# Performance work log

Hardware: AMD Instinct MI355X
Metric: run time of the kernel (lower is better)

The kernel has to match this reference:

```python
import jax, jax.numpy as jnp
from jax import lax
import numpy as np

SLOPE = 0.1  # LeakyReLU negative slope used throughout DA_conv


def setup_inputs() -> dict:
    key = jax.random.key(0)
    ks = jax.random.split(key, 8)
    B, C, H, W = 16, 64, 160, 160
    Cout, red = 64, 8
    feat = jax.random.normal(ks[0], (B, C, H, W), dtype=jnp.float32)
    deg = jax.random.normal(ks[1], (B, C, 1, 1), dtype=jnp.float32)
    W1 = jax.random.normal(ks[2], (64, C), dtype=jnp.float32) * 0.05
    W2 = jax.random.normal(ks[3], (Cout * 9, 64), dtype=jnp.float32) * 0.05
    Wc = jax.random.normal(ks[4], (Cout, Cout), dtype=jnp.float32) * 0.05
    bc = jnp.zeros((Cout,), dtype=jnp.float32)
    Wd1 = jax.random.normal(ks[5], (red, C), dtype=jnp.float32) * 0.05
    Wd2 = jax.random.normal(ks[6], (Cout, red), dtype=jnp.float32) * 0.05
    return {"feat": feat, "deg": deg, "W1": W1, "W2": W2, "Wc": Wc,
            "bc": bc, "Wd1": Wd1, "Wd2": Wd2}


def reference(feat, deg, W1, W2, Wc, bc, Wd1, Wd2):
    B, C, H, W = feat.shape
    Cout = Wc.shape[0]
    KS = 3
    d = deg[:, :, 0, 0]  # [B, C]

    # --- dynamic per-sample, per-channel 3x3 kernel generation ---
    h = jax.nn.leaky_relu(d @ W1.T, SLOPE)            # [B, 64]
    k = (h @ W2.T).reshape(B * Cout, 1, KS, KS)        # [B*Cout, 1, 3, 3]

    # grouped depthwise conv: input [1, B*C, H, W], groups = B*C
    x = feat.reshape(1, B * C, H, W)
    out = lax.conv_general_dilated(
        x, k, window_strides=(1, 1), padding=[(1, 1), (1, 1)],
        dimension_numbers=("NCHW", "OIHW", "NCHW"),
        feature_group_count=B * C)
    out = jax.nn.leaky_relu(out, SLOPE).reshape(B, Cout, H, W)

    # 1x1 conv with bias (common.default_conv)
    out = jnp.einsum("oi,bihw->bohw", Wc, out) + bc[None, :, None, None]

    # --- channel attention branch (1x1 convs == matmuls on [B,C]) ---
    a = jax.nn.leaky_relu(jnp.einsum("ri,bi->br", Wd1, d), SLOPE)   # [B, red]
    att = jax.nn.sigmoid(jnp.einsum("or,br->bo", Wd2, a))           # [B, Cout]

    return out + feat * att[:, :, None, None]
```

## Files before the change

### kernel.cpp

```cpp
#include <hip/hip_runtime.h>
#include <hip/hip_bf16.h>
#include <math.h>

#define SLOPE 0.1f
#define B_ 16
#define C_ 64
#define H_ 160
#define W_ 160
#define HW_ (H_*W_)

typedef short bf16x8 __attribute__((ext_vector_type(8)));
typedef float f32x4  __attribute__((ext_vector_type(4)));
typedef unsigned int uint2v __attribute__((ext_vector_type(2)));

__device__ __forceinline__ float lrelu(float x) { return fmaxf(x, SLOPE * x); }
__device__ __forceinline__ unsigned f2bf(float x) {
  union { float f; unsigned u; } c; c.f = x;
  return (c.u + 0x7fffu + ((c.u >> 16) & 1u)) >> 16;
}
__device__ __forceinline__ float bf2f(unsigned short u) {
  union { unsigned u; float f; } c; c.u = ((unsigned)u) << 16; return c.f;
}

__device__ __forceinline__ void gl2lds16(const void* g, void* l) {
  __builtin_amdgcn_global_load_lds(
      (const __attribute__((address_space(1))) void*)g,
      (__attribute__((address_space(3))) void*)l, 16, 0, 0);
}

__global__ __launch_bounds__(64) void prep_kernel(
    const float* __restrict__ deg,
    const float* __restrict__ W1,
    const float* __restrict__ W2,
    const float* __restrict__ Wd1,
    const float* __restrict__ Wd2,
    float* __restrict__ ws) {
  const int b = blockIdx.x;
  const int j = threadIdx.x;
  __shared__ float sd[64], sh[64], sa[8];
  sd[j] = deg[b * 64 + j];
  __syncthreads();

  float acc = 0.f;
  for (int i = 0; i < 64; ++i) acc = fmaf(sd[i], W1[j * 64 + i], acc);
  sh[j] = lrelu(acc);

  if (j < 8) {
    float s = 0.f;
    for (int i = 0; i < 64; ++i) s = fmaf(sd[i], Wd1[j * 64 + i], s);
    sa[j] = lrelu(s);
  }
  __syncthreads();

  float kv[9];
#pragma unroll
  for (int t = 0; t < 9; ++t) kv[t] = 0.f;
  for (int l = 0; l < 64; ++l) {
    float hl = sh[l];
#pragma unroll
    for (int t = 0; t < 9; ++t) kv[t] = fmaf(hl, W2[(j * 9 + t) * 64 + l], kv[t]);
  }
  const int slot = ((j & 15) >> 2) * 16 + (j >> 4) * 4 + (j & 3);
  unsigned short* kw = (unsigned short*)((char*)ws + 4096) + (b * 64 + slot) * 12;
#pragma unroll
  for (int t = 0; t < 9; ++t) kw[t] = (unsigned short)f2bf(kv[t]);
  kw[9] = 0; kw[10] = 0; kw[11] = 0;

  float s2 = 0.f;
#pragma unroll
  for (int r = 0; r < 8; ++r) s2 = fmaf(Wd2[j * 8 + r], sa[r], s2);
  ws[b * 64 + j] = 1.f / (1.f + __expf(-s2));
}

__global__ __launch_bounds__(256, 4) void main_kernel(
    const float* __restrict__ feat,
    const float* __restrict__ Wc,
    const float* __restrict__ bc,
    const float* __restrict__ ws,
    float* __restrict__ out) {
  __shared__ __align__(16) float S[2][16][244];
  __shared__ __align__(16) unsigned short Tt[2048];
  __shared__ __align__(16) unsigned short Ff[2048];
  __shared__ __align__(16) unsigned short Kl[768];

  const int rb  = blockIdx.x;
  const int bid = (rb & 7) * 400 + (rb >> 3);
  const int b   = bid / 200;
  const int rem = bid - b * 200;
  const int ty  = rem / 10, tx = rem - ty * 10;
  const int x0 = tx * 16, y0 = ty * 8;
  const int tid = threadIdx.x;
  const int lane = tid & 63, wid = tid >> 6;

  const float* __restrict__ attp  = ws + b * 64;
  const char*  __restrict__ kb8   = (const char*)ws + 4096 + b * 1536;
  const float* __restrict__ plane = feat + (size_t)(b * 64) * HW_;

  const int ci = tid >> 4;
  const int q  = (tid >> 2) & 3;
  const int h  = tid & 3;
  const int nl = lane & 15, kg = lane >> 4;
  const int ochunk = wid * 16;

  const int srow = lane / 6;
  const int schk = lane - srow * 6;
  const int grow = min(max(y0 + srow - 1, 0), H_ - 1);
  const int gcol = min(max(x0 - 4 + schk * 4, 0), W_ - 4);
  const float* sp0 = plane + grow * W_ + gcol;

  union AF { bf16x8 v; unsigned short u[8]; };
  AF a[4];
  const unsigned short ab = (unsigned short)f2bf(attp[ochunk + nl]);
#pragma unroll
  for (int g = 0; g < 4; ++g) {
    const float4 w = *(const float4*)(Wc + (ochunk + nl) * 64 + g * 16 + 4 * kg);
    a[g].u[0] = (unsigned short)f2bf(w.x); a[g].u[1] = (unsigned short)f2bf(w.y);
    a[g].u[2] = (unsigned short)f2bf(w.z); a[g].u[3] = (unsigned short)f2bf(w.w);
#pragma unroll
    for (int j = 0; j < 4; ++j)
      a[g].u[4 + j] = (wid == g && nl == 4 * kg + j) ? ab : (unsigned short)0;
  }
  const float4 bcv = *(const float4*)(bc + ochunk + 4 * kg);

  asm volatile("s_waitcnt vmcnt(0)" ::: "memory");

  if (lane < 24) gl2lds16(kb8 + wid * 384 + lane * 16, &Kl[wid * 192]);
#define STAGE(g_, bf_) \
  if (lane < 60) { \
    const float* s_ = sp0 + (size_t)((g_) * 16 + wid * 4) * HW_; \
    gl2lds16(s_,            &S[bf_][wid * 4 + 0][0]); \
    gl2lds16(s_ + HW_,      &S[bf_][wid * 4 + 1][0]); \
    gl2lds16(s_ + 2 * HW_,  &S[bf_][wid * 4 + 2][0]); \
    gl2lds16(s_ + 3 * HW_,  &S[bf_][wid * 4 + 3][0]); \
  }
  STAGE(0, 0);
  STAGE(1, 1);

  f32x4 acc[8];
#pragma unroll
  for (int nt = 0; nt < 8; ++nt) acc[nt] = (f32x4){0.f, 0.f, 0.f, 0.f};

  const float mlz = (x0 == 0 && q == 0) ? 0.f : 1.f;
  const float mrz = (x0 == W_ - 16 && q == 3) ? 0.f : 1.f;

  const unsigned t_base = (unsigned)(uintptr_t)&Tt[0] + (unsigned)(lane * 8);
  const unsigned f_base = (unsigned)(uintptr_t)&Ff[0] + (unsigned)(lane * 8);
  union BU { bf16x8 v; uint2v qv[2]; };

#pragma unroll
  for (int g = 0; g < 4; ++g) {
    const int sb = g & 1;
    if (g < 3) {
      asm volatile("s_waitcnt vmcnt(4)" ::: "memory");
    } else {
      asm volatile("s_waitcnt vmcnt(0)" ::: "memory");
    }
    __builtin_amdgcn_sched_barrier(0);

    const unsigned short* kr = &Kl[(wid * 16 + g * 4 + (lane >> 4)) * 12];
    union KU { uint2v v; unsigned short u[4]; };
    KU kA, kB;
    kA.v = *(const uint2v*)(kr);
    kB.v = *(const uint2v*)(kr + 4);
    const unsigned short k8u = kr[8];
    float kk[9];
#pragma unroll
    for (int t = 0; t < 4; ++t) { kk[t] = bf2f(kA.u[t]); kk[4 + t] = bf2f(kB.u[t]); }
    kk[8] = bf2f(k8u);

    float rv[4][9];
#pragma unroll
    for (int rr = 0; rr < 4; ++rr) {
      const float* sp = &S[sb][ci][(2 * h + rr) * 24 + 4 * q];
      const f32x4 v0 = *(const f32x4*)sp;
      const f32x4 v1 = *(const f32x4*)(sp + 4);
      rv[rr][0] = v0[0]; rv[rr][1] = v0[1]; rv[rr][2] = v0[2];
      rv[rr][3] = v0[3] * mlz;
      rv[rr][4] = v1[0]; rv[rr][5] = v1[1]; rv[rr][6] = v1[2]; rv[rr][7] = v1[3];
      rv[rr][8] = sp[8] * mrz;
    }

#pragma unroll
    for (int rr = 0; rr < 2; ++rr) {
      const int srw = 2 * h + rr;
      const float mt = (srw == 0 && y0 == 0) ? 0.f : 1.f;
      const float mb = (srw == 7 && y0 == H_ - 8) ? 0.f : 1.f;
      float sv[4], fv[4];
#pragma unroll
      for (int j = 0; j < 4; ++j) {
        float ts = fmaf(rv[rr][j + 5], kk[2], fmaf(rv[rr][j + 4], kk[1], rv[rr][j + 3] * kk[0]));
        float cs = fmaf(rv[rr + 1][j + 5], kk[5], fmaf(rv[rr + 1][j + 4], kk[4], rv[rr + 1][j + 3] * kk[3]));
        float bs = fmaf(rv[rr + 2][j + 5], kk[8], fmaf(rv[rr + 2][j + 4], kk[7], rv[rr + 2][j + 3] * kk[6]));
        sv[j] = fmaf(mt, ts, fmaf(mb, bs, cs));
        fv[j] = rv[rr + 1][j + 4];
      }
      uint2v tq, fq;
      tq.x = f2bf(lrelu(sv[0])) | (f2bf(lrelu(sv[1])) << 16);
      tq.y = f2bf(lrelu(sv[2])) | (f2bf(lrelu(sv[3])) << 16);
      fq.x = f2bf(fv[0]) | (f2bf(fv[1]) << 16);
      fq.y = f2bf(fv[2]) | (f2bf(fv[3]) << 16);
      const int tidx = srw * 256 + ci * 16 + 4 * q;
      *(uint2v*)&Tt[tidx] = tq;
      *(uint2v*)&Ff[tidx] = fq;
    }

    if (g < 2) { STAGE(g + 2, sb); }

    asm volatile("s_waitcnt lgkmcnt(0)" ::: "memory");
    __builtin_amdgcn_sched_barrier(0);
    __builtin_amdgcn_s_barrier();
    __builtin_amdgcn_sched_barrier(0);

    if (wid == g) {
      uint2v t0, t1, t2, t3, t4, t5, t6, t7;
      uint2v f0, f1, f2, f3, f4, f5, f6, f7;
      asm volatile("ds_read_b64_tr_b16 %0, %1 offset:0"    : "=v"(t0) : "v"(t_base));
      asm volatile("ds_read_b64_tr_b16 %0, %1 offset:512"  : "=v"(t1) : "v"(t_base));
      asm volatile("ds_read_b64_tr_b16 %0, %1 offset:0"    : "=v"(f0) : "v"(f_base));
      asm volatile("ds_read_b64_tr_b16 %0, %1 offset:512"  : "=v"(f1) : "v"(f_base));
      asm volatile("ds_read_b64_tr_b16 %0, %1 offset:1024" : "=v"(t2) : "v"(t_base));
      asm volatile("ds_read_b64_tr_b16 %0, %1 offset:1536" : "=v"(t3) : "v"(t_base));
      asm volatile("ds_read_b64_tr_b16 %0, %1 offset:1024" : "=v"(f2) : "v"(f_base));
      asm volatile("ds_read_b64_tr_b16 %0, %1 offset:1536" : "=v"(f3) : "v"(f_base));
      asm volatile("s_waitcnt lgkmcnt(4)" ::: "memory");
      __builtin_amdgcn_sched_barrier(0);
      {
        BU u0, u1;
        u0.qv[0] = t0; u0.qv[1] = f0;
        u1.qv[0] = t1; u1.qv[1] = f1;
        acc[0] = __builtin_amdgcn_mfma_f32_16x16x32_bf16(a[g].v, u0.v, acc[0], 0, 0, 0);
        acc[1] = __builtin_amdgcn_mfma_f32_16x16x32_bf16(a[g].v, u1.v, acc[1], 0, 0, 0);
      }
      asm volatile("ds_read_b64_tr_b16 %0, %1 offset:2048" : "=v"(t4) : "v"(t_base));
      asm volatile("ds_read_b64_tr_b16 %0, %1 offset:2560" : "=v"(t5) : "v"(t_base));
      asm volatile("ds_read_b64_tr_b16 %0, %1 offset:2048" : "=v"(f4) : "v"(f_base));
      asm volatile("ds_read_b64_tr_b16 %0, %1 offset:2560" : "=v"(f5) : "v"(f_base));
      asm volatile("s_waitcnt lgkmcnt(4)" ::: "memory");
      __builtin_amdgcn_sched_barrier(0);
      {
        BU u2, u3;
        u2.qv[0] = t2; u2.qv[1] = f2;
        u3.qv[0] = t3; u3.qv[1] = f3;
        acc[2] = __builtin_amdgcn_mfma_f32_16x16x32_bf16(a[g].v, u2.v, acc[2], 0, 0, 0);
        acc[3] = __builtin_amdgcn_mfma_f32_16x16x32_bf16(a[g].v, u3.v, acc[3], 0, 0, 0);
      }
      asm volatile("ds_read_b64_tr_b16 %0, %1 offset:3072" : "=v"(t6) : "v"(t_base));
      asm volatile("ds_read_b64_tr_b16 %0, %1 offset:3584" : "=v"(t7) : "v"(t_base));
      asm volatile("ds_read_b64_tr_b16 %0, %1 offset:3072" : "=v"(f6) : "v"(f_base));
      asm volatile("ds_read_b64_tr_b16 %0, %1 offset:3584" : "=v"(f7) : "v"(f_base));
      asm volatile("s_waitcnt lgkmcnt(4)" ::: "memory");
      __builtin_amdgcn_sched_barrier(0);
      {
        BU u4, u5;
        u4.qv[0] = t4; u4.qv[1] = f4;
        u5.qv[0] = t5; u5.qv[1] = f5;
        acc[4] = __builtin_amdgcn_mfma_f32_16x16x32_bf16(a[g].v, u4.v, acc[4], 0, 0, 0);
        acc[5] = __builtin_amdgcn_mfma_f32_16x16x32_bf16(a[g].v, u5.v, acc[5], 0, 0, 0);
      }
      asm volatile("s_waitcnt lgkmcnt(0)" ::: "memory");
      __builtin_amdgcn_sched_barrier(0);
      {
        BU u6, u7;
        u6.qv[0] = t6; u6.qv[1] = f6;
        u7.qv[0] = t7; u7.qv[1] = f7;
        acc[6] = __builtin_amdgcn_mfma_f32_16x16x32_bf16(a[g].v, u6.v, acc[6], 0, 0, 0);
        acc[7] = __builtin_amdgcn_mfma_f32_16x16x32_bf16(a[g].v, u7.v, acc[7], 0, 0, 0);
      }
    } else {
      uint2v ta0, ta1, ta2, ta3, tb0, tb1, tb2, tb3;
      asm volatile("ds_read_b64_tr_b16 %0, %1 offset:0"    : "=v"(ta0) : "v"(t_base));
      asm volatile("ds_read_b64_tr_b16 %0, %1 offset:512"  : "=v"(ta1) : "v"(t_base));
      asm volatile("ds_read_b64_tr_b16 %0, %1 offset:1024" : "=v"(ta2) : "v"(t_base));
      asm volatile("ds_read_b64_tr_b16 %0, %1 offset:1536" : "=v"(ta3) : "v"(t_base));
      asm volatile("s_waitcnt lgkmcnt(0)" ::: "memory");
      __builtin_amdgcn_sched_barrier(0);
      asm volatile("ds_read_b64_tr_b16 %0, %1 offset:2048" : "=v"(tb0) : "v"(t_base));
      asm volatile("ds_read_b64_tr_b16 %0, %1 offset:2560" : "=v"(tb1) : "v"(t_base));
      asm volatile("ds_read_b64_tr_b16 %0, %1 offset:3072" : "=v"(tb2) : "v"(t_base));
      asm volatile("ds_read_b64_tr_b16 %0, %1 offset:3584" : "=v"(tb3) : "v"(t_base));
      {
        BU u0, u1, u2, u3;
        u0.qv[0] = ta0; u0.qv[1] = (uint2v){0u, 0u};
        u1.qv[0] = ta1; u1.qv[1] = (uint2v){0u, 0u};
        u2.qv[0] = ta2; u2.qv[1] = (uint2v){0u, 0u};
        u3.qv[0] = ta3; u3.qv[1] = (uint2v){0u, 0u};
        acc[0] = __builtin_amdgcn_mfma_f32_16x16x32_bf16(a[g].v, u0.v, acc[0], 0, 0, 0);
        acc[1] = __builtin_amdgcn_mfma_f32_16x16x32_bf16(a[g].v, u1.v, acc[1], 0, 0, 0);
        acc[2] = __builtin_amdgcn_mfma_f32_16x16x32_bf16(a[g].v, u2.v, acc[2], 0, 0, 0);
        acc[3] = __builtin_amdgcn_mfma_f32_16x16x32_bf16(a[g].v, u3.v, acc[3], 0, 0, 0);
      }
      asm volatile("s_waitcnt lgkmcnt(0)" ::: "memory");
      __builtin_amdgcn_sched_barrier(0);
      {
        BU u4, u5, u6, u7;
        u4.qv[0] = tb0; u4.qv[1] = (uint2v){0u, 0u};
        u5.qv[0] = tb1; u5.qv[1] = (uint2v){0u, 0u};
        u6.qv[0] = tb2; u6.qv[1] = (uint2v){0u, 0u};
        u7.qv[0] = tb3; u7.qv[1] = (uint2v){0u, 0u};
        acc[4] = __builtin_amdgcn_mfma_f32_16x16x32_bf16(a[g].v, u4.v, acc[4], 0, 0, 0);
        acc[5] = __builtin_amdgcn_mfma_f32_16x16x32_bf16(a[g].v, u5.v, acc[5], 0, 0, 0);
        acc[6] = __builtin_amdgcn_mfma_f32_16x16x32_bf16(a[g].v, u6.v, acc[6], 0, 0, 0);
        acc[7] = __builtin_amdgcn_mfma_f32_16x16x32_bf16(a[g].v, u7.v, acc[7], 0, 0, 0);
      }
    }
    __builtin_amdgcn_s_barrier();
    __builtin_amdgcn_sched_barrier(0);
  }
#undef STAGE

  const int ob = ochunk + 4 * kg;
  float* __restrict__ outb = out + (size_t)(b * 64) * HW_;
#pragma unroll
  for (int nt = 0; nt < 8; ++nt) {
    const int off = (y0 + nt) * W_ + x0 + nl;
    outb[(size_t)(ob + 0) * HW_ + off] = acc[nt][0] + bcv.x;
    outb[(size_t)(ob + 1) * HW_ + off] = acc[nt][1] + bcv.y;
    outb[(size_t)(ob + 2) * HW_ + off] = acc[nt][2] + bcv.z;
    outb[(size_t)(ob + 3) * HW_ + off] = acc[nt][3] + bcv.w;
  }
}

extern "C" void kernel_launch(void* const* d_in, const int* in_sizes, int n_in,
                              void* d_out, int out_size, void* d_ws, size_t ws_size,
                              hipStream_t stream) {
  const float* feat = (const float*)d_in[0];
  const float* deg  = (const float*)d_in[1];
  const float* W1   = (const float*)d_in[2];
  const float* W2   = (const float*)d_in[3];
  const float* Wc   = (const float*)d_in[4];
  const float* bc   = (const float*)d_in[5];
  const float* Wd1  = (const float*)d_in[6];
  const float* Wd2  = (const float*)d_in[7];
  float* out = (float*)d_out;
  float* ws  = (float*)d_ws;

  prep_kernel<<<dim3(B_), dim3(64), 0, stream>>>(deg, W1, W2, Wd1, Wd2, ws);
  main_kernel<<<dim3(3200), dim3(256), 0, stream>>>(feat, Wc, bc, ws, out);
}
```

Measured before the change: 65.91 us.

## Double-buffer Tt/Ff LDS tiles to drop the trailing per-group barrier

Doubles the Tt and Ff transposed bf16 LDS buffers and indexes them by the stage buffer sb. The MFMA reads for one group can then overlap the next group's writes, so the barrier at the end of each loop iteration is removed. This cuts one workgroup barrier per iteration. In exchange LDS use grows, and launch bounds drop from 4 to 3 blocks per CU, which lowers occupancy. Correctness depends on sb alternating between consecutive groups so a buffer is never overwritten while another wave is still reading it.

```diff
diff --git a/kernel.cpp b/kernel.cpp
--- a/kernel.cpp
+++ b/kernel.cpp
@@ -72,15 +72,15 @@
   ws[b * 64 + j] = 1.f / (1.f + __expf(-s2));
 }
 
-__global__ __launch_bounds__(256, 4) void main_kernel(
+__global__ __launch_bounds__(256, 3) void main_kernel(
     const float* __restrict__ feat,
     const float* __restrict__ Wc,
     const float* __restrict__ bc,
     const float* __restrict__ ws,
     float* __restrict__ out) {
   __shared__ __align__(16) float S[2][16][244];
-  __shared__ __align__(16) unsigned short Tt[2048];
-  __shared__ __align__(16) unsigned short Ff[2048];
+  __shared__ __align__(16) unsigned short Tt[4096];
+  __shared__ __align__(16) unsigned short Ff[4096];
   __shared__ __align__(16) unsigned short Kl[768];
 
   const int rb  = blockIdx.x;
@@ -199,7 +199,7 @@
       tq.y = f2bf(lrelu(sv[2])) | (f2bf(lrelu(sv[3])) << 16);
       fq.x = f2bf(fv[0]) | (f2bf(fv[1]) << 16);
       fq.y = f2bf(fv[2]) | (f2bf(fv[3]) << 16);
-      const int tidx = srw * 256 + ci * 16 + 4 * q;
+      const int tidx = sb * 2048 + srw * 256 + ci * 16 + 4 * q;
       *(uint2v*)&Tt[tidx] = tq;
       *(uint2v*)&Ff[tidx] = fq;
     }
@@ -211,17 +211,20 @@
     __builtin_amdgcn_s_barrier();
     __builtin_amdgcn_sched_barrier(0);
 
+    const unsigned tb = t_base + (unsigned)(sb * 4096);
+    const unsigned fb = f_base + (unsigned)(sb * 4096);
+
     if (wid == g) {
       uint2v t0, t1, t2, t3, t4, t5, t6, t7;
       uint2v f0, f1, f2, f3, f4, f5, f6, f7;
-      asm volatile("ds_read_b64_tr_b16 %0, %1 offset:0"    : "=v"(t0) : "v"(t_base));
-      asm volatile("ds_read_b64_tr_b16 %0, %1 offset:512"  : "=v"(t1) : "v"(t_base));
-      asm volatile("ds_read_b64_tr_b16 %0, %1 offset:0"    : "=v"(f0) : "v"(f_base));
-      asm volatile("ds_read_b64_tr_b16 %0, %1 offset:512"  : "=v"(f1) : "v"(f_base));
-      asm volatile("ds_read_b64_tr_b16 %0, %1 offset:1024" : "=v"(t2) : "v"(t_base));
-      asm volatile("ds_read_b64_tr_b16 %0, %1 offset:1536" : "=v"(t3) : "v"(t_base));
-      asm volatile("ds_read_b64_tr_b16 %0, %1 offset:1024" : "=v"(f2) : "v"(f_base));
-      asm volatile("ds_read_b64_tr_b16 %0, %1 offset:1536" : "=v"(f3) : "v"(f_base));
+      asm volatile("ds_read_b64_tr_b16 %0, %1 offset:0"    : "=v"(t0) : "v"(tb));
+      asm volatile("ds_read_b64_tr_b16 %0, %1 offset:512"  : "=v"(t1) : "v"(tb));
+      asm volatile("ds_read_b64_tr_b16 %0, %1 offset:0"    : "=v"(f0) : "v"(fb));
+      asm volatile("ds_read_b64_tr_b16 %0, %1 offset:512"  : "=v"(f1) : "v"(fb));
+      asm volatile("ds_read_b64_tr_b16 %0, %1 offset:1024" : "=v"(t2) : "v"(tb));
+      asm volatile("ds_read_b64_tr_b16 %0, %1 offset:1536" : "=v"(t3) : "v"(tb));
+      asm volatile("ds_read_b64_tr_b16 %0, %1 offset:1024" : "=v"(f2) : "v"(fb));
+      asm volatile("ds_read_b64_tr_b16 %0, %1 offset:1536" : "=v"(f3) : "v"(fb));
       asm volatile("s_waitcnt lgkmcnt(4)" ::: "memory");
       __builtin_amdgcn_sched_barrier(0);
       {
@@ -231,10 +234,10 @@
         acc[0] = __builtin_amdgcn_mfma_f32_16x16x32_bf16(a[g].v, u0.v, acc[0], 0, 0, 0);
         acc[1] = __builtin_amdgcn_mfma_f32_16x16x32_bf16(a[g].v, u1.v, acc[1], 0, 0, 0);
       }
-      asm volatile("ds_read_b64_tr_b16 %0, %1 offset:2048" : "=v"(t4) : "v"(t_base));
-      asm volatile("ds_read_b64_tr_b16 %0, %1 offset:2560" : "=v"(t5) : "v"(t_base));
-      asm volatile("ds_read_b64_tr_b16 %0, %1 offset:2048" : "=v"(f4) : "v"(f_base));
-      asm volatile("ds_read_b64_tr_b16 %0, %1 offset:2560" : "=v"(f5) : "v"(f_base));
+      asm volatile("ds_read_b64_tr_b16 %0, %1 offset:2048" : "=v"(t4) : "v"(tb));
+      asm volatile("ds_read_b64_tr_b16 %0, %1 offset:2560" : "=v"(t5) : "v"(tb));
+      asm volatile("ds_read_b64_tr_b16 %0, %1 offset:2048" : "=v"(f4) : "v"(fb));
+      asm volatile("ds_read_b64_tr_b16 %0, %1 offset:2560" : "=v"(f5) : "v"(fb));
       asm volatile("s_waitcnt lgkmcnt(4)" ::: "memory");
       __builtin_amdgcn_sched_barrier(0);
       {
@@ -244,10 +247,10 @@
         acc[2] = __builtin_amdgcn_mfma_f32_16x16x32_bf16(a[g].v, u2.v, acc[2], 0, 0, 0);
         acc[3] = __builtin_amdgcn_mfma_f32_16x16x32_bf16(a[g].v, u3.v, acc[3], 0, 0, 0);
       }
-      asm volatile("ds_read_b64_tr_b16 %0, %1 offset:3072" : "=v"(t6) : "v"(t_base));
-      asm volatile("ds_read_b64_tr_b16 %0, %1 offset:3584" : "=v"(t7) : "v"(t_base));
-      asm volatile("ds_read_b64_tr_b16 %0, %1 offset:3072" : "=v"(f6) : "v"(f_base));
-      asm volatile("ds_read_b64_tr_b16 %0, %1 offset:3584" : "=v"(f7) : "v"(f_base));
+      asm volatile("ds_read_b64_tr_b16 %0, %1 offset:3072" : "=v"(t6) : "v"(tb));
+      asm volatile("ds_read_b64_tr_b16 %0, %1 offset:3584" : "=v"(t7) : "v"(tb));
+      asm volatile("ds_read_b64_tr_b16 %0, %1 offset:3072" : "=v"(f6) : "v"(fb));
+      asm volatile("ds_read_b64_tr_b16 %0, %1 offset:3584" : "=v"(f7) : "v"(fb));
       asm volatile("s_waitcnt lgkmcnt(4)" ::: "memory");
       __builtin_amdgcn_sched_barrier(0);
       {
@@ -268,16 +271,16 @@
       }
     } else {
       uint2v ta0, ta1, ta2, ta3, tb0, tb1, tb2, tb3;
-      asm volatile("ds_read_b64_tr_b16 %0, %1 offset:0"    : "=v"(ta0) : "v"(t_base));
-      asm volatile("ds_read_b64_tr_b16 %0, %1 offset:512"  : "=v"(ta1) : "v"(t_base));
-      asm volatile("ds_read_b64_tr_b16 %0, %1 offset:1024" : "=v"(ta2) : "v"(t_base));
-      asm volatile("ds_read_b64_tr_b16 %0, %1 offset:1536" : "=v"(ta3) : "v"(t_base));
+      asm volatile("ds_read_b64_tr_b16 %0, %1 offset:0"    : "=v"(ta0) : "v"(tb));
+      asm volatile("ds_read_b64_tr_b16 %0, %1 offset:512"  : "=v"(ta1) : "v"(tb));
+      asm volatile("ds_read_b64_tr_b16 %0, %1 offset:1024" : "=v"(ta2) : "v"(tb));
+      asm volatile("ds_read_b64_tr_b16 %0, %1 offset:1536" : "=v"(ta3) : "v"(tb));
       asm volatile("s_waitcnt lgkmcnt(0)" ::: "memory");
       __builtin_amdgcn_sched_barrier(0);
-      asm volatile("ds_read_b64_tr_b16 %0, %1 offset:2048" : "=v"(tb0) : "v"(t_base));
-      asm volatile("ds_read_b64_tr_b16 %0, %1 offset:2560" : "=v"(tb1) : "v"(t_base));
-      asm volatile("ds_read_b64_tr_b16 %0, %1 offset:3072" : "=v"(tb2) : "v"(t_base));
-      asm volatile("ds_read_b64_tr_b16 %0, %1 offset:3584" : "=v"(tb3) : "v"(t_base));
+      asm volatile("ds_read_b64_tr_b16 %0, %1 offset:2048" : "=v"(tb0) : "v"(tb));
+      asm volatile("ds_read_b64_tr_b16 %0, %1 offset:2560" : "=v"(tb1) : "v"(tb));
+      asm volatile("ds_read_b64_tr_b16 %0, %1 offset:3072" : "=v"(tb2) : "v"(tb));
+      asm volatile("ds_read_b64_tr_b16 %0, %1 offset:3584" : "=v"(tb3) : "v"(tb));
       {
         BU u0, u1, u2, u3;
         u0.qv[0] = ta0; u0.qv[1] = (uint2v){0u, 0u};
@@ -303,8 +306,6 @@
         acc[7] = __builtin_amdgcn_mfma_f32_16x16x32_bf16(a[g].v, u7.v, acc[7], 0, 0, 0);
       }
     }
-    __builtin_amdgcn_s_barrier();
-    __builtin_amdgcn_sched_barrier(0);
   }
 #undef STAGE
 
```

Result: no change. 66.96 us (+1.6%).
